# Kernel tuning notes

Measured on AMD Instinct MI355X. Metric: run time of the kernel, lower is better.

The kernel has to match this reference:

```python
import jax, jax.numpy as jnp
import numpy as np
from jax import lax

EPS = 1e-10
DELU_P = 10.0

def delu(x):
    # delu_feature_map: param*relu(x) + (exp(param*min(x,0)) - 1) + 1
    x1 = jax.nn.relu(x)
    x2 = jnp.exp(DELU_P * (x - x1)) - 1.0
    return DELU_P * x1 + x2 + 1.0

def conv1x1(x, w, b):
    # x: (B,C,H,W), w: (O,C), b: (O,)
    return jnp.einsum('bchw,oc->bohw', x, w) + b[None, :, None, None]

def conv3x3(x, w, b):
    # w: (O,I,3,3), SAME padding, stride 1
    y = lax.conv_general_dilated(x, w, window_strides=(1, 1), padding='SAME',
                                 dimension_numbers=('NCHW', 'OIHW', 'NCHW'))
    return y + b[None, :, None, None]

def setup_inputs() -> dict:
    key = jax.random.key(0)
    ks = jax.random.split(key, 12)
    B, C, H, W = 4, 256, 128, 128
    s = 0.02
    return {
        'x':   jax.random.normal(ks[0], (B, C, H, W), dtype=jnp.float32),
        'wq':  jax.random.normal(ks[1], (C, C), dtype=jnp.float32) * s,
        'bq':  jax.random.normal(ks[2], (C,), dtype=jnp.float32) * s,
        'wk':  jax.random.normal(ks[3], (C, C), dtype=jnp.float32) * s,
        'bk':  jax.random.normal(ks[4], (C,), dtype=jnp.float32) * s,
        'wv':  jax.random.normal(ks[5], (C, C), dtype=jnp.float32) * s,
        'bv':  jax.random.normal(ks[6], (C,), dtype=jnp.float32) * s,
        'wd1': jax.random.normal(ks[7], (C, C), dtype=jnp.float32) * s,
        'bd1': jax.random.normal(ks[8], (C,), dtype=jnp.float32) * s,
        'wd3': jax.random.normal(ks[9], (C, C, 3, 3), dtype=jnp.float32) * s,
        'bd3': jax.random.normal(ks[10], (C,), dtype=jnp.float32) * s,
        'gamma': jax.random.normal(ks[11], (1,), dtype=jnp.float32) * 0.1,
    }

def reference(x, wq, bq, wk, bk, wv, bv, wd1, bd1, wd3, bd3, gamma):
    B, C, H, W = x.shape
    N = H * W
    # q/k/v projections flattened to (B, C, N)
    q = conv1x1(x, wq, bq).reshape(B, C, N)
    k = conv1x1(x, wk, bk).reshape(B, C, N)
    v = conv1x1(x, wv, bv).reshape(B, C, N)
    # feature maps (torch permutes q to (B,N,C), applies map, permutes back -> elementwise, no-op layout)
    q = delu(q)
    k = delu(k)
    # energy: (B, C, C), contracting over spatial N (q indexed 'bmn')
    energy = jnp.einsum('bmn,bcn->bmc', q, k)
    KV = k * v  # (B, C, N) elementwise
    norm = 1.0 / (jnp.einsum('bmc,bcn->bn', energy, k) + EPS)  # (B, N)
    # attention: sum over m of energy, times KV, times norm -> (B, C, N)
    attention = jnp.einsum('bmc,bcn,bn->bcn', energy, KV, norm)
    out = attention.reshape(B, C, H, W)
    out = out + conv1x1(x, wd1, bd1) + conv3x3(x, wd3, bd3)
    return x + gamma[0] * out
```

## Files before the change

### kernel.cpp

```cpp
#include <hip/hip_runtime.h>
#include <hip/hip_fp8.h>

#define BB 4
#define CC 256
#define HH 128
#define WW 128
#define NN (HH*WW)
#define EPSF 1e-10f

#define XR 130
#define XPB ((size_t)XR*XR*CC)

typedef __bf16 bf16x8 __attribute__((ext_vector_type(8)));
typedef float  f32x4  __attribute__((ext_vector_type(4)));
typedef float  f32x16 __attribute__((ext_vector_type(16)));
typedef unsigned char uchar;

__device__ __forceinline__ float delu_f(float v) {
    return v > 0.0f ? fmaf(10.0f, v, 1.0f) : __expf(10.0f * v);
}

__device__ __forceinline__ uchar fp8b(float f) { return __hip_fp8_e4m3(f).__x; }
__device__ __forceinline__ float fp8f(uchar v) { __hip_fp8_e4m3 t; t.__x = v; return (float)t; }

__device__ __forceinline__ void gl_lds16(const void* g, void* l) {
    __builtin_amdgcn_global_load_lds(
        (const __attribute__((address_space(1))) void*)g,
        (__attribute__((address_space(3))) void*)l, 16, 0, 0);
}

__global__ __launch_bounds__(256) void k_prep(const float* __restrict__ wq,
    const float* __restrict__ wk, const float* __restrict__ wv,
    const float* __restrict__ wd1, const float* __restrict__ wd3,
    __bf16* __restrict__ wqb, __bf16* __restrict__ wkb, __bf16* __restrict__ wvb,
    uchar* __restrict__ wcv8)
{
    int idx = blockIdx.x * 256 + threadIdx.x;
    if (idx >= CC*CC) return;
    const int oc = idx >> 8, ic = idx & 255;
    const int ocf32 = oc >> 5;
    const int gks = ic >> 4, khi = (ic >> 3) & 1;
    const int lane32 = khi*32 + (oc & 31);
    const int e = ic & 7;
    const size_t off32 = ((size_t)(gks*8 + ocf32)*64 + lane32)*8 + e;
    wqb[off32] = (__bf16)wq[idx];
    wkb[off32] = (__bf16)wk[idx];
    wvb[off32] = (__bf16)wv[idx];
    float w9[9];
    #pragma unroll
    for (int k=0;k<9;k++) w9[k] = wd3[(size_t)idx*9 + k];
    w9[4] += wd1[idx];
    #pragma unroll
    for (int t=0;t<9;t++) wcv8[(size_t)t*CC*CC + off32] = fp8b(w9[t] * 16.0f);
}

__global__ __launch_bounds__(256) void k_halo(__bf16* __restrict__ xpad,
                                              uchar* __restrict__ xpad8)
{
    const int b = blockIdx.y;
    for (int t = blockIdx.x*256 + threadIdx.x; t < 516*32; t += 256*gridDim.x) {
        const int icg = t & 31;
        const int p   = t >> 5;
        int xrow, xcol;
        if (p < 260)      { xrow = (p < 130) ? 0 : 129; xcol = p % 130; }
        else              { int q = p - 260; xrow = 1 + (q >> 1); xcol = (q & 1) ? 129 : 0; }
        const size_t off = (size_t)b*XPB + ((size_t)xrow*XR + xcol)*CC + icg*8;
        *(bf16x8*)&xpad[off] = (bf16x8){};
        *(unsigned long long*)&xpad8[off] = 0ull;
    }
}

__device__ __forceinline__ void stage_row128(const __bf16* __restrict__ xrb,
                                             __bf16* __restrict__ xs,
                                             int wid, int lane)
{
    #pragma unroll
    for (int j = 0; j < 16; ++j) {
        const int it = wid + 4*j;
        const int kq = it >> 1, ch = it & 1;
        gl_lds16(xrb + (size_t)(ch*64 + lane)*CC + kq*8, &xs[(size_t)(kq*132 + ch*64)*8]);
    }
}

__device__ __forceinline__ void mfma_gemm32(const __bf16* __restrict__ wb,
                                            const __bf16* __restrict__ xs,
                                            int wid, int lane, int l31, int lhi,
                                            f32x16 acc[2][4])
{
    #pragma unroll
    for (int kb=0; kb<8; kb++) {
        bf16x8 af[4];
        #pragma unroll
        for (int f=0; f<2; f++)
            #pragma unroll
            for (int kk=0; kk<2; kk++)
                af[f*2+kk] = *(const bf16x8*)&wb[((size_t)((kb*2+kk)*8 + wid*2 + f)*64 + lane)*8];
        #pragma unroll
        for (int kk=0; kk<2; kk++)
            #pragma unroll
            for (int nf=0; nf<4; nf++) {
                bf16x8 br = *(const bf16x8*)&xs[(size_t)((kb*4 + kk*2 + lhi)*132 + nf*32 + l31)*8];
                #pragma unroll
                for (int f=0; f<2; f++)
                    acc[f][nf] = __builtin_amdgcn_mfma_f32_32x32x16_bf16(af[f*2+kk], br, acc[f][nf], 0, 0, 0);
            }
    }
}

__global__ __launch_bounds__(256) void k_qk_mfma(const float* __restrict__ x,
    const __bf16* __restrict__ wqb, const float* __restrict__ bq,
    const __bf16* __restrict__ wkb, const float* __restrict__ bk,
    uchar* __restrict__ kp8, float* __restrict__ Qs,
    __bf16* __restrict__ xpad, uchar* __restrict__ xpad8)
{
    __shared__ __bf16 xs[32*132*8];
    __shared__ float Qpart[4][128];
    const int h  = blockIdx.x;
    const int n0 = h * 128;
    const int b  = blockIdx.y;
    const int tid = threadIdx.x;
    const int wid = tid >> 6, lane = tid & 63;
    const int l31 = lane & 31, lhi = lane >> 5;
    const int oc_base = wid*64;

    const float* xb = x + (size_t)b*CC*NN + (size_t)h*WW;
    {
        const int ic7 = tid & 7;
        const int col = ((tid >> 3) & 31) * 4;
        #pragma unroll
        for (int i = 0; i < 32; ++i) {
            const int ic = i*8 + ic7;
            float4 v = *(const float4*)&xb[(size_t)ic*NN + col];
            const int b0 = (i*132 + col)*8 + ic7;
            xs[b0]      = (__bf16)v.x;
            xs[b0 + 8]  = (__bf16)v.y;
            xs[b0 + 16] = (__bf16)v.z;
            xs[b0 + 24] = (__bf16)v.w;
        }
    }
    __syncthreads();

    {
        __bf16* xpb  = xpad  + (size_t)b*XPB + ((size_t)(h+1)*XR + 1)*CC;
        uchar*  xpb8 = xpad8 + (size_t)b*XPB + ((size_t)(h+1)*XR + 1)*CC;
        #pragma unroll
        for (int it = 0; it < 16; ++it) {
            const int o   = it*256 + tid;
            const int col = o >> 5, kq = o & 31;
            bf16x8 v = *(const bf16x8*)&xs[(size_t)(kq*132 + col)*8];
            unsigned long long pk = 0;
            #pragma unroll
            for (int j = 0; j < 8; ++j)
                pk |= ((unsigned long long)fp8b((float)v[j])) << (8*j);
            *(bf16x8*)&xpb[(size_t)col*CC + kq*8] = v;
            *(unsigned long long*)&xpb8[(size_t)col*CC + kq*8] = pk;
        }
    }

    f32x16 acc[2][4] = {};
    mfma_gemm32(wqb, xs, wid, lane, l31, lhi, acc);
    #pragma unroll
    for (int nf=0; nf<4; nf++) {
        float s = 0.0f;
        #pragma unroll
        for (int f=0; f<2; f++)
            #pragma unroll
            for (int reg=0; reg<16; reg++) {
                const int oc = oc_base + f*32 + (reg&3) + 8*(reg>>2) + 4*lhi;
                s += delu_f(acc[f][nf][reg] + bq[oc]);
            }
        s += __shfl_xor(s, 32);
        if (lhi == 0) Qpart[wid][nf*32 + l31] = s;
    }
    __syncthreads();
    if (tid < 128)
        Qs[(size_t)b*NN + n0 + tid] = Qpart[0][tid] + Qpart[1][tid] + Qpart[2][tid] + Qpart[3][tid];

    #pragma unroll
    for (int f=0; f<2; f++)
        #pragma unroll
        for (int nf=0; nf<4; nf++)
            acc[f][nf] = (f32x16){};
    mfma_gemm32(wkb, xs, wid, lane, l31, lhi, acc);
    #pragma unroll
    for (int f=0; f<2; f++) {
        #pragma unroll
        for (int reg=0; reg<16; reg++) {
            const int oc = oc_base + f*32 + (reg&3) + 8*(reg>>2) + 4*lhi;
            const float bias = bk[oc];
            uchar* kr = kp8 + ((size_t)b*CC + oc)*NN + n0;
            #pragma unroll
            for (int nf=0; nf<4; nf++)
                kr[nf*32 + l31] = fp8b(delu_f(acc[f][nf][reg] + bias));
        }
    }
}

__global__ __launch_bounds__(256) void k_esum(const uchar* __restrict__ kp8,
    const float* __restrict__ Qs, float* __restrict__ Es)
{
    const int c = blockIdx.x & (CC-1), b = blockIdx.x >> 8;
    const int tid = threadIdx.x;
    const uchar* kr = kp8 + ((size_t)b*CC + c)*NN;
    const float4* qr = (const float4*)(Qs + (size_t)b*NN);
    float s = 0.0f;
    for (int i = tid; i < NN/8; i += 256) {
        unsigned long long kkb = *(const unsigned long long*)&kr[(size_t)i*8];
        float4 q0 = qr[2*i], q1 = qr[2*i+1];
        const float qv[8] = {q0.x,q0.y,q0.z,q0.w,q1.x,q1.y,q1.z,q1.w};
        #pragma unroll
        for (int j=0;j<8;j++)
            s = fmaf(fp8f((uchar)(kkb >> (8*j))), qv[j], s);
    }
    #pragma unroll
    for (int m=1; m<64; m<<=1) s += __shfl_xor(s, m, 64);
    __shared__ float red[4];
    if ((tid & 63) == 0) red[tid >> 6] = s;
    __syncthreads();
    if (tid == 0) Es[b*CC + c] = red[0] + red[1] + red[2] + red[3];
}

__global__ __launch_bounds__(256,2) void k_conv_mfma(const uchar* __restrict__ xpad8,
    const uchar* __restrict__ wcv8, const float* __restrict__ bd1,
    const float* __restrict__ bd3, __bf16* __restrict__ convout)
{
    __shared__ uchar xs8[2][6*132*16];
    const int orig = blockIdx.x;
    const int wg   = (orig & 7)*64 + (orig >> 3);
    const int b    = wg >> 7;
    const int h    = wg & 127;
    const int tid = threadIdx.x;
    const int wid = tid >> 6, lane = tid & 63;
    const int l31 = lane & 31, lhi = lane >> 5;
    const int oc_base = wid*64;
    const uchar* xpb8 = xpad8 + (size_t)b*XPB;

    f32x16 acc[2][4] = {};

    #define STAGE_CV8(bufsel, icb) do {                                         \
        const int ic0_ = (icb)*32;                                              \
        _Pragma("unroll")                                                       \
        for (int j = 0; j < 5; ++j) {                                           \
            const int w_ = wid + 4*j;                                           \
            if (w_ < 18) {                                                      \
                const int pair_ = w_ / 3, chunk_ = w_ % 3;                      \
                const int r_ = pair_ >> 1, g16_ = pair_ & 1;                    \
                const int col0_ = chunk_ * 64;                                  \
                if (col0_ + lane < XR)                                          \
                    gl_lds16(xpb8 + ((size_t)(h + r_)*XR + col0_ + lane)*CC + ic0_ + g16_*16, \
                             &xs8[bufsel][(size_t)(pair_*132 + col0_)*16]);     \
            }                                                                   \
        }                                                                       \
    } while (0)

    #define AF8_LOAD(dst, t, icb)                                               \
        _Pragma("unroll")                                                       \
        for (int f=0; f<2; f++)                                                 \
            _Pragma("unroll")                                                   \
            for (int kk=0; kk<2; kk++)                                          \
                dst[f*2+kk] = *(const long*)&wcv8[(size_t)(t)*CC*CC +           \
                    ((size_t)((((icb)*2 + kk)*8 + wid*2 + f))*64 + lane)*8];

    STAGE_CV8(0, 0);
    __syncthreads();

    #pragma unroll 1
    for (int icb = 0; icb < 8; ++icb) {
        long af8[2][4];
        AF8_LOAD(af8[0], 0, icb);
        if (icb < 7) STAGE_CV8((icb+1)&1, icb+1);
        #pragma unroll
        for (int t=0; t<9; ++t) {
            const int cur = t & 1, nxt = cur ^ 1;
            const int ky = t/3, kx = t%3;
            if (t < 8) { AF8_LOAD(af8[nxt], t+1, icb); }
            __builtin_amdgcn_s_setprio(1);
            #pragma unroll
            for (int kk=0; kk<2; kk++) {
                #pragma unroll
                for (int nf=0; nf<4; nf++) {
                    long br = *(const long*)&xs8[icb & 1][
                        (size_t)((ky*2 + kk)*132 + nf*32 + l31 + kx)*16 + lhi*8];
                    #pragma unroll
                    for (int f=0; f<2; f++)
                        acc[f][nf] = __builtin_amdgcn_mfma_f32_32x32x16_fp8_fp8(
                            af8[cur][f*2+kk], br, acc[f][nf], 0, 0, 0);
                }
            }
            __builtin_amdgcn_s_setprio(0);
        }
        __syncthreads();
    }
    #undef STAGE_CV8
    #undef AF8_LOAD

    #pragma unroll
    for (int f=0; f<2; f++) {
        #pragma unroll
        for (int reg=0; reg<16; reg++) {
            const int row = (reg & 3) + 8*(reg >> 2) + 4*lhi;
            const int oc = oc_base + f*32 + row;
            const float bias = bd1[oc] + bd3[oc];
            __bf16* orow = convout + ((size_t)b*CC + oc)*NN + (size_t)h*WW;
            #pragma unroll
            for (int nf=0; nf<4; nf++) {
                const int w = nf*32 + l31;
                orow[w] = (__bf16)(acc[f][nf][reg]*0.0625f + bias);
            }
        }
    }
}

__global__ __launch_bounds__(256) void k_vattn_mfma(
    const __bf16* __restrict__ xpad,
    const __bf16* __restrict__ wvb, const float* __restrict__ bv,
    const uchar* __restrict__ kp8, const float* __restrict__ Es,
    const __bf16* __restrict__ convout,
    const float* __restrict__ gamma, float* __restrict__ out)
{
    __shared__ __bf16 xs[32*132*8];
    __shared__ float Dpart[4][128];
    __shared__ float rn_sh[128];
    const int h  = blockIdx.x;
    const int n0 = h * 128;
    const int b  = blockIdx.y;
    const int tid = threadIdx.x;
    const int wid = tid >> 6, lane = tid & 63;
    const int l31 = lane & 31, lhi = lane >> 5;
    const int oc_base = wid*64;
    const __bf16* xrb = xpad + (size_t)b*XPB + ((size_t)(h+1)*XR + 1)*CC;

    stage_row128(xrb, xs, wid, lane);
    __syncthreads();

    f32x16 acc[2][4] = {};
    mfma_gemm32(wvb, xs, wid, lane, l31, lhi, acc);

    float dpart[4] = {0.f,0.f,0.f,0.f};
    #pragma unroll
    for (int f=0; f<2; f++) {
        #pragma unroll
        for (int reg=0; reg<16; reg++) {
            const int oc = oc_base + f*32 + (reg&3) + 8*(reg>>2) + 4*lhi;
            const float e = Es[b*CC + oc];
            const uchar* kr = kp8 + ((size_t)b*CC + oc)*NN + n0;
            #pragma unroll
            for (int nf=0; nf<4; nf++)
                dpart[nf] = fmaf(e, fp8f(kr[nf*32 + l31]), dpart[nf]);
        }
    }
    #pragma unroll
    for (int nf=0; nf<4; nf++) {
        dpart[nf] += __shfl_xor(dpart[nf], 32);
        if (lhi == 0) Dpart[wid][nf*32 + l31] = dpart[nf];
    }
    __syncthreads();
    if (tid < 128)
        rn_sh[tid] = 1.0f / (Dpart[0][tid] + Dpart[1][tid] + Dpart[2][tid] + Dpart[3][tid] + EPSF);
    __syncthreads();

    const float g = gamma[0];
    #pragma unroll
    for (int f=0; f<2; f++) {
        #pragma unroll
        for (int reg=0; reg<16; reg++) {
            const int oc = oc_base + f*32 + (reg&3) + 8*(reg>>2) + 4*lhi;
            const float eg = Es[b*CC + oc] * g;
            const float bias = bv[oc];
            const uchar*  kr = kp8 + ((size_t)b*CC + oc)*NN + n0;
            const __bf16* cr = convout + ((size_t)b*CC + oc)*NN + n0;
            const __bf16* xr = &xs[(size_t)((oc >> 3)*132)*8 + (oc & 7)];
            float* orow = out + ((size_t)b*CC + oc)*NN + n0;
            #pragma unroll
            for (int nf=0; nf<4; nf++) {
                const int w = nf*32 + l31;
                const float attn = eg*fp8f(kr[w])*rn_sh[w]*(acc[f][nf][reg] + bias);
                const float xv = (float)xr[(size_t)w*8];
                orow[w] = xv + attn + g*(float)cr[w];
            }
        }
    }
}

extern "C" void kernel_launch(void* const* d_in, const int* in_sizes, int n_in,
                              void* d_out, int out_size, void* d_ws, size_t ws_size,
                              hipStream_t stream)
{
    const float* x     = (const float*)d_in[0];
    const float* wq    = (const float*)d_in[1];
    const float* bq    = (const float*)d_in[2];
    const float* wk    = (const float*)d_in[3];
    const float* bk    = (const float*)d_in[4];
    const float* wv    = (const float*)d_in[5];
    const float* bv    = (const float*)d_in[6];
    const float* wd1   = (const float*)d_in[7];
    const float* bd1   = (const float*)d_in[8];
    const float* wd3   = (const float*)d_in[9];
    const float* bd3   = (const float*)d_in[10];
    const float* gamma = (const float*)d_in[11];
    float* out = (float*)d_out;

    uchar*  kp8   = (uchar*)d_ws;
    __bf16* cvout = (__bf16*)(kp8 + (size_t)BB*CC*NN);
    float*  Qs    = (float*)(cvout + (size_t)BB*CC*NN);
    float*  Es    = Qs + (size_t)BB*NN;
    uchar*  wcv8  = (uchar*)(Es + (size_t)BB*CC);
    __bf16* wqb   = (__bf16*)(wcv8 + (size_t)9*CC*CC);
    __bf16* wkb   = wqb + (size_t)CC*CC;
    __bf16* wvb   = wkb + (size_t)CC*CC;
    __bf16* xpad  = wvb + (size_t)CC*CC;
    uchar*  xpad8 = (uchar*)(xpad + (size_t)BB*XPB);

    k_prep      <<<dim3(CC*CC/256), 256, 0, stream>>>(wq, wk, wv, wd1, wd3, wqb, wkb, wvb, wcv8);
    k_halo      <<<dim3(16, BB), 256, 0, stream>>>(xpad, xpad8);
    k_qk_mfma   <<<dim3(HH, BB), 256, 0, stream>>>(x, wqb, bq, wkb, bk, kp8, Qs, xpad, xpad8);
    k_esum      <<<dim3(BB*CC), 256, 0, stream>>>(kp8, Qs, Es);
    k_conv_mfma <<<dim3(HH*BB), 256, 0, stream>>>(xpad8, wcv8, bd1, bd3, cvout);
    k_vattn_mfma<<<dim3(HH, BB), 256, 0, stream>>>(xpad, wvb, bv, kp8, Es, cvout, gamma, out);
}
```

Before: 164.7 us.

## Merge prep/halo and conv/esum launches, store conv output as fp8

Merges the weight-prep and halo-zeroing kernels into one launch. Interleaves the E-sum reduction blocks with the 3x3 conv blocks in a single grid so the two independent workloads overlap and one launch is removed. The conv intermediate is stored as fp8 e4m3 instead of bf16, halving its write and read traffic. The fp8 storage lowers the precision of the conv term added to the output.

```diff
diff --git a/kernel.cpp b/kernel.cpp
--- a/kernel.cpp
+++ b/kernel.cpp
@@ -29,14 +29,30 @@
         (__attribute__((address_space(3))) void*)l, 16, 0, 0);
 }
 
-__global__ __launch_bounds__(256) void k_prep(const float* __restrict__ wq,
+__global__ __launch_bounds__(256) void k_prep_halo(const float* __restrict__ wq,
     const float* __restrict__ wk, const float* __restrict__ wv,
     const float* __restrict__ wd1, const float* __restrict__ wd3,
     __bf16* __restrict__ wqb, __bf16* __restrict__ wkb, __bf16* __restrict__ wvb,
-    uchar* __restrict__ wcv8)
-{
-    int idx = blockIdx.x * 256 + threadIdx.x;
-    if (idx >= CC*CC) return;
+    uchar* __restrict__ wcv8,
+    __bf16* __restrict__ xpad, uchar* __restrict__ xpad8)
+{
+    const int bi = blockIdx.x;
+    if (bi >= CC*CC/256) {
+        const int sub = bi - CC*CC/256;
+        const int b = sub >> 4;
+        for (int t = (sub & 15)*256 + threadIdx.x; t < 516*32; t += 256*16) {
+            const int icg = t & 31;
+            const int p   = t >> 5;
+            int xrow, xcol;
+            if (p < 260)      { xrow = (p < 130) ? 0 : 129; xcol = p % 130; }
+            else              { int q = p - 260; xrow = 1 + (q >> 1); xcol = (q & 1) ? 129 : 0; }
+            const size_t off = (size_t)b*XPB + ((size_t)xrow*XR + xcol)*CC + icg*8;
+            *(bf16x8*)&xpad[off] = (bf16x8){};
+            *(unsigned long long*)&xpad8[off] = 0ull;
+        }
+        return;
+    }
+    int idx = bi * 256 + threadIdx.x;
     const int oc = idx >> 8, ic = idx & 255;
     const int ocf32 = oc >> 5;
     const int gks = ic >> 4, khi = (ic >> 3) & 1;
@@ -54,22 +70,6 @@
     for (int t=0;t<9;t++) wcv8[(size_t)t*CC*CC + off32] = fp8b(w9[t] * 16.0f);
 }
 
-__global__ __launch_bounds__(256) void k_halo(__bf16* __restrict__ xpad,
-                                              uchar* __restrict__ xpad8)
-{
-    const int b = blockIdx.y;
-    for (int t = blockIdx.x*256 + threadIdx.x; t < 516*32; t += 256*gridDim.x) {
-        const int icg = t & 31;
-        const int p   = t >> 5;
-        int xrow, xcol;
-        if (p < 260)      { xrow = (p < 130) ? 0 : 129; xcol = p % 130; }
-        else              { int q = p - 260; xrow = 1 + (q >> 1); xcol = (q & 1) ? 129 : 0; }
-        const size_t off = (size_t)b*XPB + ((size_t)xrow*XR + xcol)*CC + icg*8;
-        *(bf16x8*)&xpad[off] = (bf16x8){};
-        *(unsigned long long*)&xpad8[off] = 0ull;
-    }
-}
-
 __device__ __forceinline__ void stage_row128(const __bf16* __restrict__ xrb,
                                              __bf16* __restrict__ xs,
                                              int wid, int lane)
@@ -196,40 +196,43 @@
     }
 }
 
-__global__ __launch_bounds__(256) void k_esum(const uchar* __restrict__ kp8,
-    const float* __restrict__ Qs, float* __restrict__ Es)
-{
-    const int c = blockIdx.x & (CC-1), b = blockIdx.x >> 8;
+__global__ __launch_bounds__(256,2) void k_conv_esum(const uchar* __restrict__ xpad8,
+    const uchar* __restrict__ wcv8, const float* __restrict__ bd1,
+    const float* __restrict__ bd3, uchar* __restrict__ convout8,
+    const uchar* __restrict__ kp8, const float* __restrict__ Qs,
+    float* __restrict__ Es)
+{
+    __shared__ uchar xs8[2][6*132*16];
+    const int bi = blockIdx.x;
     const int tid = threadIdx.x;
-    const uchar* kr = kp8 + ((size_t)b*CC + c)*NN;
-    const float4* qr = (const float4*)(Qs + (size_t)b*NN);
-    float s = 0.0f;
-    for (int i = tid; i < NN/8; i += 256) {
-        unsigned long long kkb = *(const unsigned long long*)&kr[(size_t)i*8];
-        float4 q0 = qr[2*i], q1 = qr[2*i+1];
-        const float qv[8] = {q0.x,q0.y,q0.z,q0.w,q1.x,q1.y,q1.z,q1.w};
-        #pragma unroll
-        for (int j=0;j<8;j++)
-            s = fmaf(fp8f((uchar)(kkb >> (8*j))), qv[j], s);
-    }
-    #pragma unroll
-    for (int m=1; m<64; m<<=1) s += __shfl_xor(s, m, 64);
-    __shared__ float red[4];
-    if ((tid & 63) == 0) red[tid >> 6] = s;
-    __syncthreads();
-    if (tid == 0) Es[b*CC + c] = red[0] + red[1] + red[2] + red[3];
-}
-
-__global__ __launch_bounds__(256,2) void k_conv_mfma(const uchar* __restrict__ xpad8,
-    const uchar* __restrict__ wcv8, const float* __restrict__ bd1,
-    const float* __restrict__ bd3, __bf16* __restrict__ convout)
-{
-    __shared__ uchar xs8[2][6*132*16];
-    const int orig = blockIdx.x;
+
+    if (bi % 3 != 0) {
+        __shared__ float red[4];
+        const int ei = (bi/3)*2 + (bi%3) - 1;
+        const int c = ei & (CC-1), b = ei >> 8;
+        const uchar* kr = kp8 + ((size_t)b*CC + c)*NN;
+        const float4* qr = (const float4*)(Qs + (size_t)b*NN);
+        float s = 0.0f;
+        for (int i = tid; i < NN/8; i += 256) {
+            unsigned long long kkb = *(const unsigned long long*)&kr[(size_t)i*8];
+            float4 q0 = qr[2*i], q1 = qr[2*i+1];
+            const float qv[8] = {q0.x,q0.y,q0.z,q0.w,q1.x,q1.y,q1.z,q1.w};
+            #pragma unroll
+            for (int j=0;j<8;j++)
+                s = fmaf(fp8f((uchar)(kkb >> (8*j))), qv[j], s);
+        }
+        #pragma unroll
+        for (int m=1; m<64; m<<=1) s += __shfl_xor(s, m, 64);
+        if ((tid & 63) == 0) red[tid >> 6] = s;
+        __syncthreads();
+        if (tid == 0) Es[b*CC + c] = red[0] + red[1] + red[2] + red[3];
+        return;
+    }
+
+    const int orig = bi / 3;
     const int wg   = (orig & 7)*64 + (orig >> 3);
     const int b    = wg >> 7;
     const int h    = wg & 127;
-    const int tid = threadIdx.x;
     const int wid = tid >> 6, lane = tid & 63;
     const int l31 = lane & 31, lhi = lane >> 5;
     const int oc_base = wid*64;
@@ -301,11 +304,11 @@
             const int row = (reg & 3) + 8*(reg >> 2) + 4*lhi;
             const int oc = oc_base + f*32 + row;
             const float bias = bd1[oc] + bd3[oc];
-            __bf16* orow = convout + ((size_t)b*CC + oc)*NN + (size_t)h*WW;
+            uchar* orow = convout8 + ((size_t)b*CC + oc)*NN + (size_t)h*WW;
             #pragma unroll
             for (int nf=0; nf<4; nf++) {
                 const int w = nf*32 + l31;
-                orow[w] = (__bf16)(acc[f][nf][reg]*0.0625f + bias);
+                orow[w] = fp8b(acc[f][nf][reg]*0.0625f + bias);
             }
         }
     }
@@ -315,7 +318,7 @@
     const __bf16* __restrict__ xpad,
     const __bf16* __restrict__ wvb, const float* __restrict__ bv,
     const uchar* __restrict__ kp8, const float* __restrict__ Es,
-    const __bf16* __restrict__ convout,
+    const uchar* __restrict__ convout8,
     const float* __restrict__ gamma, float* __restrict__ out)
 {
     __shared__ __bf16 xs[32*132*8];
@@ -367,8 +370,8 @@
             const int oc = oc_base + f*32 + (reg&3) + 8*(reg>>2) + 4*lhi;
             const float eg = Es[b*CC + oc] * g;
             const float bias = bv[oc];
-            const uchar*  kr = kp8 + ((size_t)b*CC + oc)*NN + n0;
-            const __bf16* cr = convout + ((size_t)b*CC + oc)*NN + n0;
+            const uchar* kr = kp8 + ((size_t)b*CC + oc)*NN + n0;
+            const uchar* cr = convout8 + ((size_t)b*CC + oc)*NN + n0;
             const __bf16* xr = &xs[(size_t)((oc >> 3)*132)*8 + (oc & 7)];
             float* orow = out + ((size_t)b*CC + oc)*NN + n0;
             #pragma unroll
@@ -376,7 +379,7 @@
                 const int w = nf*32 + l31;
                 const float attn = eg*fp8f(kr[w])*rn_sh[w]*(acc[f][nf][reg] + bias);
                 const float xv = (float)xr[(size_t)w*8];
-                orow[w] = xv + attn + g*(float)cr[w];
+                orow[w] = xv + attn + g*fp8f(cr[w]);
             }
         }
     }
@@ -400,21 +403,21 @@
     const float* gamma = (const float*)d_in[11];
     float* out = (float*)d_out;
 
-    uchar*  kp8   = (uchar*)d_ws;
-    __bf16* cvout = (__bf16*)(kp8 + (size_t)BB*CC*NN);
-    float*  Qs    = (float*)(cvout + (size_t)BB*CC*NN);
-    float*  Es    = Qs + (size_t)BB*NN;
-    uchar*  wcv8  = (uchar*)(Es + (size_t)BB*CC);
-    __bf16* wqb   = (__bf16*)(wcv8 + (size_t)9*CC*CC);
-    __bf16* wkb   = wqb + (size_t)CC*CC;
-    __bf16* wvb   = wkb + (size_t)CC*CC;
-    __bf16* xpad  = wvb + (size_t)CC*CC;
-    uchar*  xpad8 = (uchar*)(xpad + (size_t)BB*XPB);
-
-    k_prep      <<<dim3(CC*CC/256), 256, 0, stream>>>(wq, wk, wv, wd1, wd3, wqb, wkb, wvb, wcv8);
-    k_halo      <<<dim3(16, BB), 256, 0, stream>>>(xpad, xpad8);
+    uchar*  kp8    = (uchar*)d_ws;
+    uchar*  cvout8 = kp8 + (size_t)BB*CC*NN;
+    float*  Qs     = (float*)(cvout8 + (size_t)BB*CC*NN);
+    float*  Es     = Qs + (size_t)BB*NN;
+    uchar*  wcv8   = (uchar*)(Es + (size_t)BB*CC);
+    __bf16* wqb    = (__bf16*)(wcv8 + (size_t)9*CC*CC);
+    __bf16* wkb    = wqb + (size_t)CC*CC;
+    __bf16* wvb    = wkb + (size_t)CC*CC;
+    __bf16* xpad   = wvb + (size_t)CC*CC;
+    uchar*  xpad8  = (uchar*)(xpad + (size_t)BB*XPB);
+
+    k_prep_halo <<<dim3(CC*CC/256 + 16*BB), 256, 0, stream>>>(
+                    wq, wk, wv, wd1, wd3, wqb, wkb, wvb, wcv8, xpad, xpad8);
     k_qk_mfma   <<<dim3(HH, BB), 256, 0, stream>>>(x, wqb, bq, wkb, bk, kp8, Qs, xpad, xpad8);
-    k_esum      <<<dim3(BB*CC), 256, 0, stream>>>(kp8, Qs, Es);
-    k_conv_mfma <<<dim3(HH*BB), 256, 0, stream>>>(xpad8, wcv8, bd1, bd3, cvout);
-    k_vattn_mfma<<<dim3(HH, BB), 256, 0, stream>>>(xpad, wvb, bv, kp8, Es, cvout, gamma, out);
-}
+    k_conv_esum <<<dim3(3*HH*BB), 256, 0, stream>>>(xpad8, wcv8, bd1, bd3, cvout8,
+                                                    kp8, Qs, Es);
+    k_vattn_mfma<<<dim3(HH, BB), 256, 0, stream>>>(xpad, wvb, bv, kp8, Es, cvout8, gamma, out);
+}
```

New measurement: 186.2 us. +13.0%, slower.
